# Optimization experiments

Measured on AMD Instinct MI355X. Metric: run time of the kernel, lower is better.

The kernel has to match this reference:

```python
import math
import jax, jax.numpy as jnp
from jax import lax
import numpy as np

B, S2, D = 8, 1024, 768  # seq_len = 32*32 spatial tokens
HD = 64                   # head_dim
K = 7                     # LocalRmsNorm kernel_size
EPS = 1e-7


def setup_inputs() -> dict:
    key = jax.random.key(0)
    ks = jax.random.split(key, 6)
    sc = 0.02
    return {
        "x": jax.random.normal(ks[0], (B, S2, D), jnp.float32),
        "norm_w": jnp.ones((D,), jnp.float32),
        "wq": jax.random.normal(ks[1], (D, D), jnp.float32) * sc,
        "bq": jnp.zeros((D,), jnp.float32),
        "wk": jax.random.normal(ks[2], (D, D), jnp.float32) * sc,
        "bk": jnp.zeros((D,), jnp.float32),
        "wv": jax.random.normal(ks[3], (D, D), jnp.float32) * sc,
        "bv": jnp.zeros((D,), jnp.float32),
        "wo": jax.random.normal(ks[4], (D, D), jnp.float32) * sc,
        "bo": jnp.zeros((D,), jnp.float32),
    }


def local_rms_norm(x, w):
    # x: [b, s*s, d]; sliding KxK box-sum of squares over the s x s grid,
    # zero-padded (matches F.unfold), mean divisor is always K*K.
    b, ss, d = x.shape
    s = int(math.isqrt(ss))
    sq = (x * x).reshape(b, s, s, d)
    box = lax.reduce_window(sq, 0.0, lax.add,
                            (1, K, K, 1), (1, 1, 1, 1), 'SAME')
    rms = jnp.sqrt(EPS + box / (K * K)).reshape(b, ss, d)
    return x / rms * w


def reference(x, norm_w, wq, bq, wk, bk, wv, bv, wo, bo):
    xn = local_rms_norm(x, norm_w)
    b, s, d = xn.shape
    h = d // HD

    def proj(w_, b_):
        return (xn @ w_.T + b_).reshape(b, s, h, HD).transpose(0, 2, 1, 3)

    q = proj(wq, bq)  # [b, h, s, dh]
    k = proj(wk, bk)
    v = proj(wv, bv)
    scores = jnp.einsum('bhqd,bhkd->bhqk', q, k) / math.sqrt(HD)
    attn = jax.nn.softmax(scores, axis=-1)
    out = jnp.einsum('bhqk,bhkd->bhqd', attn, v)
    out = out.transpose(0, 2, 1, 3).reshape(b, s, d)
    return out @ wo.T + bo
```

## Files before the change

kernel.cpp:

```cpp
#include <hip/hip_runtime.h>

typedef _Float16 f16x8 __attribute__((ext_vector_type(8)));
typedef _Float16 f16x4 __attribute__((ext_vector_type(4)));
typedef _Float16 f16x2 __attribute__((ext_vector_type(2)));
typedef float    f32x4 __attribute__((ext_vector_type(4)));
typedef float    f32x16 __attribute__((ext_vector_type(16)));
typedef unsigned int u32x4 __attribute__((ext_vector_type(4)));
typedef unsigned short ushort_t;
typedef unsigned int uint_t;

#define LOG2E 1.44269504088896340736f

#define CFENCE  asm volatile("" ::: "memory")
#define HWBAR   __builtin_amdgcn_s_barrier()
#define VMCNT0  asm volatile("s_waitcnt vmcnt(0)" ::: "memory")
#define VMCNT3  asm volatile("s_waitcnt vmcnt(3)" ::: "memory")
#define VMCNT4  asm volatile("s_waitcnt vmcnt(4)" ::: "memory")

__device__ __forceinline__ ushort_t f2h(float x) {
  _Float16 h = (_Float16)x;
  return __builtin_bit_cast(ushort_t, h);
}

__device__ __forceinline__ float fexp2(float x) {
#if __has_builtin(__builtin_amdgcn_exp2f)
  return __builtin_amdgcn_exp2f(x);
#else
  float r; asm("v_exp_f32 %0, %1" : "=v"(r) : "v"(x)); return r;
#endif
}

__device__ __forceinline__ float frsq(float x) {
#if __has_builtin(__builtin_amdgcn_rsqf)
  return __builtin_amdgcn_rsqf(x);
#else
  float r; asm("v_rsq_f32 %0, %1" : "=v"(r) : "v"(x)); return r;
#endif
}

__device__ __forceinline__ uint_t packpair(float a, float b) {
  return __builtin_bit_cast(uint_t, __builtin_amdgcn_cvt_pkrtz(a, b));
}

__device__ __forceinline__ f16x8 mk8(uint_t a, uint_t b, uint_t c, uint_t d) {
  u32x4 t; t[0] = a; t[1] = b; t[2] = c; t[3] = d;
  return __builtin_bit_cast(f16x8, t);
}

__device__ __forceinline__ void gload_lds16(const void* g, void* lds) {
  __builtin_amdgcn_global_load_lds(
      (const __attribute__((address_space(1))) void*)(uintptr_t)g,
      (__attribute__((address_space(3))) void*)(unsigned)(uintptr_t)lds,
      16, 0, 0);
}


__global__ __launch_bounds__(256)
void lrn_a(const float* __restrict__ x, ushort_t* __restrict__ tmp) {
  int tid = blockIdx.x * 256 + threadIdx.x;
  int dv  = tid % 192;
  int rem = tid / 192;
  int pos = rem & 1023;
  int b   = rem >> 10;
  int r = pos >> 5, c = pos & 31;
  const float4* base = (const float4*)x + ((size_t)b * 1024 + (size_t)r * 32) * 192 + dv;
  float ax = 0.f, ay = 0.f, az = 0.f, aw = 0.f;
#pragma unroll
  for (int dc = -3; dc <= 3; ++dc) {
    int cc = c + dc;
    if (cc >= 0 && cc < 32) {
      float4 v = base[cc * 192];
      ax += v.x * v.x; ay += v.y * v.y; az += v.z * v.z; aw += v.w * v.w;
    }
  }
  f16x4 o;
  o[0] = (_Float16)ax; o[1] = (_Float16)ay; o[2] = (_Float16)az; o[3] = (_Float16)aw;
  *(f16x4*)(tmp + (size_t)tid * 4) = o;
}

__global__ __launch_bounds__(256)
void lrn_b(const float* __restrict__ x, const ushort_t* __restrict__ tmp,
           const float* __restrict__ wn, ushort_t* __restrict__ xn) {
  int tid = blockIdx.x * 256 + threadIdx.x;
  int dv  = tid % 192;
  int rem = tid / 192;
  int pos = rem & 1023;
  int b   = rem >> 10;
  int r = pos >> 5, c = pos & 31;
  const ushort_t* tb = tmp + (((size_t)b * 1024 + c) * 192 + dv) * 4;
  float ax = 0.f, ay = 0.f, az = 0.f, aw = 0.f;
#pragma unroll
  for (int dr = -3; dr <= 3; ++dr) {
    int rr = r + dr;
    if (rr >= 0 && rr < 32) {
      f16x4 v = *(const f16x4*)(tb + (size_t)rr * 24576);
      ax += (float)v[0]; ay += (float)v[1]; az += (float)v[2]; aw += (float)v[3];
    }
  }
  float4 xv = ((const float4*)x)[tid];
  float4 wv = ((const float4*)wn)[dv];
  const float inv49 = 1.0f / 49.0f;
  float i0 = frsq(1e-7f + ax * inv49);
  float i1 = frsq(1e-7f + ay * inv49);
  float i2 = frsq(1e-7f + az * inv49);
  float i3 = frsq(1e-7f + aw * inv49);
  f16x4 o;
  o[0] = (_Float16)(xv.x * i0 * wv.x);
  o[1] = (_Float16)(xv.y * i1 * wv.y);
  o[2] = (_Float16)(xv.z * i2 * wv.z);
  o[3] = (_Float16)(xv.w * i3 * wv.w);
  const int m = b * 1024 + pos;
  const int panel = m >> 4, lrr = m & 15;
  const int kc = dv >> 3, lg2 = (dv >> 1) & 3, half = dv & 1;
  *(f16x4*)(xn + ((size_t)((panel * 24 + kc) * 64 + lg2 * 16 + lrr)) * 8 + half * 4) = o;
}

__global__ __launch_bounds__(256)
void convw_fm(const float* __restrict__ wq, const float* __restrict__ wk,
              const float* __restrict__ wv, const float* __restrict__ wo,
              ushort_t* __restrict__ bqkv, ushort_t* __restrict__ bwo) {
  const int g = blockIdx.x * 256 + threadIdx.x;
  const int mat = g / 73728;
  const int gg = g % 73728;
  const int panel = gg / 1536;
  const int rem = gg % 1536;
  const int kc = rem >> 6, l = rem & 63;
  const int row = panel * 16 + (l & 15);
  const int col = kc * 32 + (l >> 4) * 8;
  const float* src = (mat == 0) ? wq : (mat == 1) ? wk : (mat == 2) ? wv : wo;
  const float4 v0 = *(const float4*)(src + (size_t)row * 768 + col);
  const float4 v1 = *(const float4*)(src + (size_t)row * 768 + col + 4);
  f16x8 o;
  o[0]=(_Float16)v0.x; o[1]=(_Float16)v0.y; o[2]=(_Float16)v0.z; o[3]=(_Float16)v0.w;
  o[4]=(_Float16)v1.x; o[5]=(_Float16)v1.y; o[6]=(_Float16)v1.z; o[7]=(_Float16)v1.w;
  if (mat < 3) *(f16x8*)(bqkv + (size_t)g * 8) = o;
  else         *(f16x8*)(bwo  + (size_t)gg * 8) = o;
}

#define GSTAGE(BUF, KT) do {                                                      \
    _Pragma("unroll")                                                             \
    for (int j = 0; j < SI; ++j)                                                  \
      gload_lds16(sb[j] + (KT) * 512, (BUF) ? d1[j] : d0[j]);                     \
  } while (0)

#define GTILE(KT, CUR, NXT) do {                                                  \
    CFENCE; HWBAR; CFENCE;                              \
    if ((KT) + 1 < 24) {                                                          \
      GSTAGE(NXT, (KT) + 1);                                                      \
      if constexpr (SI == 4) VMCNT4; else VMCNT3;       \
    } else VMCNT0;                                                                \
    CFENCE; HWBAR;                                \
    __builtin_amdgcn_sched_barrier(0);                                            \
    f16x8 af[MT], bf[NT];                                                         \
    _Pragma("unroll")                                                             \
    for (int mt = 0; mt < MT; ++mt)                                               \
      af[mt] = *(const f16x8*)(&As[CUR][(wr * MT + mt) * 512 + l * 8]);           \
    _Pragma("unroll")                                                             \
    for (int nt = 0; nt < NT; ++nt)                                               \
      bf[nt] = *(const f16x8*)(&Bs[CUR][(wc * NT + nt) * 512 + l * 8]);           \
    _Pragma("unroll")                                                             \
    for (int mt = 0; mt < MT; ++mt)                                               \
      _Pragma("unroll")                                                           \
      for (int nt = 0; nt < NT; ++nt)                                             \
        acc[mt][nt] = __builtin_amdgcn_mfma_f32_16x16x32_f16(af[mt], bf[nt], acc[mt][nt], 0, 0, 0); \
  } while (0)

template <int MODE>
__global__ __launch_bounds__(256)
void gemm_lds(const ushort_t* __restrict__ Afm, const ushort_t* __restrict__ Bfm,
              const float* __restrict__ b0, const float* __restrict__ b1,
              const float* __restrict__ b2,
              ushort_t* __restrict__ q, ushort_t* __restrict__ k,
              ushort_t* __restrict__ v, float* __restrict__ outf) {
  constexpr int PM  = (MODE == 0) ? 8 : 4;
  constexpr int PN  = 8;
  constexpr int NBN = (MODE == 0) ? 18 : 6;
  constexpr int SI  = (PM + PN) / 4;
  constexpr int MT  = PM / 2, NT = PN / 2;
  __shared__ __align__(16) ushort_t As[2][PM * 512];
  __shared__ __align__(16) ushort_t Bs[2][PN * 512];

  const int nwg = gridDim.x;
  const int bid = blockIdx.x;
  const int cid = (bid & 7) * (nwg >> 3) + (bid >> 3);
  const int bm = cid / NBN, bn = cid % NBN;
  const int tid = threadIdx.x;
  const int w = tid >> 6, l = tid & 63;
  const int wr = w >> 1, wc = w & 1;
  const int lr = l & 15, lg = l >> 4;

  f32x4 acc[MT][NT] = {};

  const ushort_t* sb[SI];
  ushort_t* d0[SI];
  ushort_t* d1[SI];
#pragma unroll
  for (int j = 0; j < SI; ++j) {
    const int g = w * SI + j;
    if (g < PM) {
      sb[j] = Afm + ((size_t)(bm * PM + g) * 24) * 512 + l * 8;
      d0[j] = &As[0][g * 512]; d1[j] = &As[1][g * 512];
    } else {
      sb[j] = Bfm + ((size_t)(bn * PN + (g - PM)) * 24) * 512 + l * 8;
      d0[j] = &Bs[0][(g - PM) * 512]; d1[j] = &Bs[1][(g - PM) * 512];
    }
  }

  GSTAGE(0, 0);
  for (int kt = 0; kt < 24; kt += 2) {
    GTILE(kt, 0, 1);
    GTILE(kt + 1, 1, 0);
  }

#pragma unroll
  for (int mt = 0; mt < MT; ++mt) {
#pragma unroll
    for (int nt = 0; nt < NT; ++nt) {
      if (MODE == 0) {
        const int n = bn * 128 + wc * 64 + nt * 16 + lr;
        const int mbase = bm * 128 + wr * 64 + mt * 16 + lg * 4;
        const int region = n / 768;
        const int nn = n - region * 768;
        const int hh = nn >> 6, hd = nn & 63;
        const float bb = (region == 0 ? b0 : region == 1 ? b1 : b2)[nn];
        if (region == 2) {
          const int bi = mbase >> 10, s0 = mbase & 1023;
          const int tile = s0 >> 6, q6 = s0 & 63;
          const int aa = q6 >> 5, r5 = q6 & 31;
          const int t1 = r5 >> 3, h2 = (r5 >> 2) & 1;
          const int gq = t1 >> 1, jj = (2 * t1) & 3;
          const int s0p = (tile << 6) + (((aa << 1) + gq) << 4) + (h2 << 3) + 2 * jj;
          f16x4 pv;
#pragma unroll
          for (int gi = 0; gi < 4; ++gi) pv[gi] = (_Float16)(acc[mt][nt][gi] + bb);
          *(f16x4*)(v + (((size_t)(bi * 12 + hh)) * 64 + hd) * 1024 + s0p) = pv;
        } else {
#pragma unroll
          for (int gi = 0; gi < 4; ++gi) {
            const int m = mbase + gi;
            const int bi = m >> 10, s = m & 1023;
            const float val = acc[mt][nt][gi] + bb;
            if (region == 0)
              q[(((size_t)(bi * 12 + hh)) * 1024 + s) * 64 + hd] = f2h(val * (0.125f * LOG2E));
            else
              k[(((size_t)(bi * 12 + hh)) * 1024 + s) * 64 + hd] = f2h(val);
          }
        }
      } else {
        const int n = bn * 128 + wc * 64 + nt * 16 + lr;
        const float bb = b0[n];
#pragma unroll
        for (int gi = 0; gi < 4; ++gi) {
          const int m = bm * 64 + wr * 32 + mt * 16 + lg * 4 + gi;
          outf[(size_t)m * 768 + n] = acc[mt][nt][gi] + bb;
        }
      }
    }
  }
}

#define ATILE(T, CUR, NXT) do {                                                   \
    CFENCE; HWBAR; CFENCE;                              \
    if ((T) < 15) {                                                               \
      const int kv0n = ((T) + 1) << 6;                                            \
      gload_lds16(kp + (size_t)(kv0n + r1) * 64 + s1 * 8,  Kl0 + (NXT) * 8192);   \
      gload_lds16(kp + (size_t)(kv0n + r2) * 64 + s2 * 8,  Kl1 + (NXT) * 8192);   \
      gload_lds16(vp + (size_t)r1 * 1024 + kv0n + s1 * 8,  Vl0 + (NXT) * 8192);   \
      gload_lds16(vp + (size_t)r2 * 1024 + kv0n + s2 * 8,  Vl1 + (NXT) * 8192);   \
      VMCNT4;                                        \
    } else VMCNT0;                                                                \
    CFENCE; HWBAR;                            \
    __builtin_amdgcn_sched_barrier(0);                                            \
    const char* kbase = (const char*)smem + (CUR) * 8192;                         \
    const char* vbase = (const char*)smem + 16384 + (CUR) * 8192;                 \
    f16x8 ka0[4], ka1[4];                                                         \
    _Pragma("unroll")                                                             \
    for (int kc = 0; kc < 4; ++kc) {                                              \
      ka0[kc] = *(const f16x8*)(kbase + off[kc]);                                 \
      ka1[kc] = *(const f16x8*)(kbase + off[kc] + 4096);                          \
    }                                                                             \
    f32x16 s0v = {}, s1v = {};                                                    \
    __builtin_amdgcn_s_setprio(1);                                                \
    _Pragma("unroll")                                                             \
    for (int kc = 0; kc < 4; ++kc) {                                              \
      s0v = __builtin_amdgcn_mfma_f32_32x32x16_f16(ka0[kc], qf[kc], s0v, 0, 0, 0);\
      s1v = __builtin_amdgcn_mfma_f32_32x32x16_f16(ka1[kc], qf[kc], s1v, 0, 0, 0);\
    }                                                                             \
    __builtin_amdgcn_s_setprio(0);                                                \
    f16x8 va0[4], va1[4];                                                         \
    _Pragma("unroll")                                                             \
    for (int c = 0; c < 4; ++c) {                                                 \
      va0[c] = *(const f16x8*)(vbase + off[c]);                                   \
      va1[c] = *(const f16x8*)(vbase + off[c] + 4096);                            \
    }                                                                             \
    uint_t pk0[8], pk1[8];                                                        \
    _Pragma("unroll")                                                             \
    for (int tt = 0; tt < 8; ++tt) {                                              \
      pk0[tt] = packpair(fexp2(s0v[2 * tt]), fexp2(s0v[2 * tt + 1]));             \
      pk1[tt] = packpair(fexp2(s1v[2 * tt]), fexp2(s1v[2 * tt + 1]));             \
    }                                                                             \
    _Pragma("unroll")                                                             \
    for (int tt = 0; tt < 4; ++tt) {                                              \
      lr0 = __builtin_amdgcn_fdot2(__builtin_bit_cast(f16x2, pk0[tt]),     one2, lr0, false); \
      lr1 = __builtin_amdgcn_fdot2(__builtin_bit_cast(f16x2, pk0[tt + 4]), one2, lr1, false); \
      lr2 = __builtin_amdgcn_fdot2(__builtin_bit_cast(f16x2, pk1[tt]),     one2, lr2, false); \
      lr3 = __builtin_amdgcn_fdot2(__builtin_bit_cast(f16x2, pk1[tt + 4]), one2, lr3, false); \
    }                                                                             \
    const f16x8 pb0 = mk8(pk0[0], pk0[1], pk0[2], pk0[3]);                        \
    const f16x8 pb1 = mk8(pk0[4], pk0[5], pk0[6], pk0[7]);                        \
    const f16x8 pb2 = mk8(pk1[0], pk1[1], pk1[2], pk1[3]);                        \
    const f16x8 pb3 = mk8(pk1[4], pk1[5], pk1[6], pk1[7]);                        \
    __builtin_amdgcn_s_setprio(1);                                                \
    oacc0 = __builtin_amdgcn_mfma_f32_32x32x16_f16(va0[0], pb0, oacc0, 0, 0, 0);  \
    oacc1 = __builtin_amdgcn_mfma_f32_32x32x16_f16(va1[0], pb0, oacc1, 0, 0, 0);  \
    oacc0 = __builtin_amdgcn_mfma_f32_32x32x16_f16(va0[1], pb1, oacc0, 0, 0, 0);  \
    oacc1 = __builtin_amdgcn_mfma_f32_32x32x16_f16(va1[1], pb1, oacc1, 0, 0, 0);  \
    oacc0 = __builtin_amdgcn_mfma_f32_32x32x16_f16(va0[2], pb2, oacc0, 0, 0, 0);  \
    oacc1 = __builtin_amdgcn_mfma_f32_32x32x16_f16(va1[2], pb2, oacc1, 0, 0, 0);  \
    oacc0 = __builtin_amdgcn_mfma_f32_32x32x16_f16(va0[3], pb3, oacc0, 0, 0, 0);  \
    oacc1 = __builtin_amdgcn_mfma_f32_32x32x16_f16(va1[3], pb3, oacc1, 0, 0, 0);  \
    __builtin_amdgcn_s_setprio(0);                                                \
  } while (0)

__global__ __launch_bounds__(256, 3)
void attn_fused10(const ushort_t* __restrict__ qb, const ushort_t* __restrict__ kb,
                  const ushort_t* __restrict__ vt, ushort_t* __restrict__ ao) {
  __shared__ __align__(16) ushort_t smem[16384];
  const int tid = threadIdx.x;
  const int w = tid >> 6, l = tid & 63;
  const int lq = l & 31, hi = l >> 5;

  const int bid = blockIdx.x;
  const int cid = (bid & 7) * 96 + (bid >> 3);
  const int bh = cid >> 3, qt = cid & 7;
  const int b = bh / 12, h = bh % 12;

  const ushort_t* qp = qb + ((size_t)bh * 1024 + qt * 128 + w * 32) * 64;
  const ushort_t* kp = kb + (size_t)bh * 65536;
  const ushort_t* vp = vt + (size_t)bh * 65536;

  f16x8 qf[4];
#pragma unroll
  for (int kc = 0; kc < 4; ++kc)
    qf[kc] = *(const f16x8*)(qp + lq * 64 + kc * 16 + hi * 8);

  const int r1 = tid >> 3,          s1 = (tid & 7) ^ (r1 & 7);
  const int r2 = (tid + 256) >> 3,  s2 = (tid & 7) ^ (r2 & 7);
  char* Kl0 = (char*)smem + w * 1024;
  char* Kl1 = (char*)smem + 4096 + w * 1024;
  char* Vl0 = (char*)smem + 16384 + w * 1024;
  char* Vl1 = (char*)smem + 16384 + 4096 + w * 1024;

  const int cswz = lq & 7;
  int off[4];
#pragma unroll
  for (int kc = 0; kc < 4; ++kc)
    off[kc] = lq * 128 + (((kc * 2 + hi) ^ cswz) * 16);

  f32x16 oacc0 = {}, oacc1 = {};
  float lr0 = 0.f, lr1 = 0.f, lr2 = 0.f, lr3 = 0.f;
  const f16x2 one2 = {(_Float16)1.f, (_Float16)1.f};

  gload_lds16(kp + (size_t)r1 * 64 + s1 * 8,   Kl0);
  gload_lds16(kp + (size_t)r2 * 64 + s2 * 8,   Kl1);
  gload_lds16(vp + (size_t)r1 * 1024 + s1 * 8, Vl0);
  gload_lds16(vp + (size_t)r2 * 1024 + s2 * 8, Vl1);

  for (int t2 = 0; t2 < 16; t2 += 2) {
    ATILE(t2, 0, 1);
    ATILE(t2 + 1, 1, 0);
  }

  float lrun = (lr0 + lr1) + (lr2 + lr3);
  lrun += __shfl_xor(lrun, 32, 64);
  const float invl = 1.0f / lrun;

  __syncthreads();

  uint_t* ot = (uint_t*)smem + w * 1024 + lq * 32;
#pragma unroll
  for (int tt = 0; tt < 8; ++tt) {
    const int base = (tt & 1) + ((tt >> 1) << 2) + 2 * hi;
    ot[base ^ lq]        = packpair(oacc0[2 * tt] * invl, oacc0[2 * tt + 1] * invl);
    ot[(base + 16) ^ lq] = packpair(oacc1[2 * tt] * invl, oacc1[2 * tt + 1] * invl);
  }
  __syncthreads();
  const int row = tid >> 1, halfc = tid & 1;
  const int w2 = row >> 5, qq = row & 31;
  const uint_t* srcp = (const uint_t*)smem + w2 * 1024 + qq * 32;
  const int m = b * 1024 + qt * 128 + row;
  const int panel = m >> 4, lrr = m & 15;
  const int kc = h * 2 + halfc;
#pragma unroll
  for (int jj = 0; jj < 4; ++jj) {
    u32x4 tv;
#pragma unroll
    for (int i2 = 0; i2 < 4; ++i2)
      tv[i2] = srcp[(halfc * 16 + jj * 4 + i2) ^ qq];
    *(u32x4*)(ao + ((size_t)((panel * 24 + kc) * 64 + jj * 16 + lrr)) * 8) = tv;
  }
}

extern "C" void kernel_launch(void* const* d_in, const int* in_sizes, int n_in,
                              void* d_out, int out_size, void* d_ws, size_t ws_size,
                              hipStream_t stream) {
  const float* x  = (const float*)d_in[0];
  const float* nw = (const float*)d_in[1];
  const float* wq = (const float*)d_in[2];
  const float* bq = (const float*)d_in[3];
  const float* wk = (const float*)d_in[4];
  const float* bk = (const float*)d_in[5];
  const float* wv = (const float*)d_in[6];
  const float* bv = (const float*)d_in[7];
  const float* wo = (const float*)d_in[8];
  const float* bo = (const float*)d_in[9];
  float* out = (float*)d_out;

  char* ws = (char*)d_ws;
  ushort_t* tmp   = (ushort_t*)ws;
  ushort_t* qbuf  = (ushort_t*)(ws);
  ushort_t* kbuf  = (ushort_t*)(ws + 12582912);
  ushort_t* xnf   = (ushort_t*)(ws + 25165824);
  ushort_t* bwqkv = (ushort_t*)(ws + 37748736);
  ushort_t* bwo   = (ushort_t*)(ws + 41287680);
  ushort_t* vtb   = (ushort_t*)(ws + 42467328);
  ushort_t* aoutf = (ushort_t*)(ws + 55050240);

  lrn_a<<<6144, 256, 0, stream>>>(x, tmp);
  lrn_b<<<6144, 256, 0, stream>>>(x, tmp, nw, xnf);
  convw_fm<<<1152, 256, 0, stream>>>(wq, wk, wv, wo, bwqkv, bwo);
  gemm_lds<0><<<1152, 256, 0, stream>>>(xnf, bwqkv, bq, bk, bv,
                                        qbuf, kbuf, vtb, nullptr);
  attn_fused10<<<768, 256, 0, stream>>>(qbuf, kbuf, vtb, aoutf);
  gemm_lds<1><<<768, 256, 0, stream>>>(aoutf, bwo, bo, nullptr, nullptr,
                                       nullptr, nullptr, nullptr, out);
}
```

Baseline: 137.9 us.

## Load GEMM B operand directly into registers instead of staging through LDS

The projection GEMMs no longer stage the weight (B) tiles in shared memory. Each wave loads its own B fragments straight from global memory into double-buffered registers, while A keeps its LDS double buffer. This cuts LDS traffic and shared-memory footprint, which may let more blocks fit per CU. The cost is duplicated global reads of B across the two wave rows, more vector registers, and revised vmcnt wait counts.

```diff
diff --git a/kernel.cpp b/kernel.cpp
--- a/kernel.cpp
+++ b/kernel.cpp
@@ -14,8 +14,9 @@
 #define CFENCE  asm volatile("" ::: "memory")
 #define HWBAR   __builtin_amdgcn_s_barrier()
 #define VMCNT0  asm volatile("s_waitcnt vmcnt(0)" ::: "memory")
-#define VMCNT3  asm volatile("s_waitcnt vmcnt(3)" ::: "memory")
 #define VMCNT4  asm volatile("s_waitcnt vmcnt(4)" ::: "memory")
+#define VMCNT5  asm volatile("s_waitcnt vmcnt(5)" ::: "memory")
+#define VMCNT6  asm volatile("s_waitcnt vmcnt(6)" ::: "memory")
 
 __device__ __forceinline__ ushort_t f2h(float x) {
   _Float16 h = (_Float16)x;
@@ -137,48 +138,51 @@
   else         *(f16x8*)(bwo  + (size_t)gg * 8) = o;
 }
 
-#define GSTAGE(BUF, KT) do {                                                      \
-    _Pragma("unroll")                                                             \
-    for (int j = 0; j < SI; ++j)                                                  \
+#define GSTAGE_A(BUF, KT) do {                                                    \
+    _Pragma("unroll")                                                             \
+    for (int j = 0; j < SIA; ++j)                                                 \
       gload_lds16(sb[j] + (KT) * 512, (BUF) ? d1[j] : d0[j]);                     \
   } while (0)
 
-#define GTILE(KT, CUR, NXT) do {                                                  \
-    CFENCE; HWBAR; CFENCE;                              \
+#define GLOADB(BREG, KT) do {                                                     \
+    _Pragma("unroll")                                                             \
+    for (int nt = 0; nt < NT; ++nt)                                               \
+      BREG[nt] = *(const f16x8*)(pb[nt] + (size_t)(KT) * 512);                    \
+  } while (0)
+
+#define GTILE(KT, CUR, NXT, BCUR, BNXT) do {                                      \
+    CFENCE; HWBAR; CFENCE;                          \
     if ((KT) + 1 < 24) {                                                          \
-      GSTAGE(NXT, (KT) + 1);                                                      \
-      if constexpr (SI == 4) VMCNT4; else VMCNT3;       \
+      GSTAGE_A(NXT, (KT) + 1);                                                    \
+      GLOADB(BNXT, (KT) + 1);                                                     \
+      if constexpr (SIA == 2) VMCNT6; else VMCNT5;           \
     } else VMCNT0;                                                                \
-    CFENCE; HWBAR;                                \
+    CFENCE; HWBAR;                              \
     __builtin_amdgcn_sched_barrier(0);                                            \
-    f16x8 af[MT], bf[NT];                                                         \
+    f16x8 af[MT];                                                                 \
     _Pragma("unroll")                                                             \
     for (int mt = 0; mt < MT; ++mt)                                               \
       af[mt] = *(const f16x8*)(&As[CUR][(wr * MT + mt) * 512 + l * 8]);           \
-    _Pragma("unroll")                                                             \
-    for (int nt = 0; nt < NT; ++nt)                                               \
-      bf[nt] = *(const f16x8*)(&Bs[CUR][(wc * NT + nt) * 512 + l * 8]);           \
     _Pragma("unroll")                                                             \
     for (int mt = 0; mt < MT; ++mt)                                               \
       _Pragma("unroll")                                                           \
       for (int nt = 0; nt < NT; ++nt)                                             \
-        acc[mt][nt] = __builtin_amdgcn_mfma_f32_16x16x32_f16(af[mt], bf[nt], acc[mt][nt], 0, 0, 0); \
+        acc[mt][nt] = __builtin_amdgcn_mfma_f32_16x16x32_f16(af[mt], BCUR[nt], acc[mt][nt], 0, 0, 0); \
   } while (0)
 
 template <int MODE>
 __global__ __launch_bounds__(256)
-void gemm_lds(const ushort_t* __restrict__ Afm, const ushort_t* __restrict__ Bfm,
-              const float* __restrict__ b0, const float* __restrict__ b1,
-              const float* __restrict__ b2,
-              ushort_t* __restrict__ q, ushort_t* __restrict__ k,
-              ushort_t* __restrict__ v, float* __restrict__ outf) {
+void gemm_breg(const ushort_t* __restrict__ Afm, const ushort_t* __restrict__ Bfm,
+               const float* __restrict__ b0, const float* __restrict__ b1,
+               const float* __restrict__ b2,
+               ushort_t* __restrict__ q, ushort_t* __restrict__ k,
+               ushort_t* __restrict__ v, float* __restrict__ outf) {
   constexpr int PM  = (MODE == 0) ? 8 : 4;
   constexpr int PN  = 8;
   constexpr int NBN = (MODE == 0) ? 18 : 6;
-  constexpr int SI  = (PM + PN) / 4;
+  constexpr int SIA = PM / 4;
   constexpr int MT  = PM / 2, NT = PN / 2;
   __shared__ __align__(16) ushort_t As[2][PM * 512];
-  __shared__ __align__(16) ushort_t Bs[2][PN * 512];
 
   const int nwg = gridDim.x;
   const int bid = blockIdx.x;
@@ -191,25 +195,26 @@
 
   f32x4 acc[MT][NT] = {};
 
-  const ushort_t* sb[SI];
-  ushort_t* d0[SI];
-  ushort_t* d1[SI];
-#pragma unroll
-  for (int j = 0; j < SI; ++j) {
-    const int g = w * SI + j;
-    if (g < PM) {
-      sb[j] = Afm + ((size_t)(bm * PM + g) * 24) * 512 + l * 8;
-      d0[j] = &As[0][g * 512]; d1[j] = &As[1][g * 512];
-    } else {
-      sb[j] = Bfm + ((size_t)(bn * PN + (g - PM)) * 24) * 512 + l * 8;
-      d0[j] = &Bs[0][(g - PM) * 512]; d1[j] = &Bs[1][(g - PM) * 512];
-    }
-  }
-
-  GSTAGE(0, 0);
+  const ushort_t* sb[SIA];
+  ushort_t* d0[SIA];
+  ushort_t* d1[SIA];
+#pragma unroll
+  for (int j = 0; j < SIA; ++j) {
+    const int g = w * SIA + j;
+    sb[j] = Afm + ((size_t)(bm * PM + g) * 24) * 512 + l * 8;
+    d0[j] = &As[0][g * 512]; d1[j] = &As[1][g * 512];
+  }
+  const ushort_t* pb[NT];
+#pragma unroll
+  for (int nt = 0; nt < NT; ++nt)
+    pb[nt] = Bfm + ((size_t)(bn * PN + wc * NT + nt) * 24) * 512 + l * 8;
+
+  f16x8 bfA[NT], bfB[NT];
+  GSTAGE_A(0, 0);
+  GLOADB(bfA, 0);
   for (int kt = 0; kt < 24; kt += 2) {
-    GTILE(kt, 0, 1);
-    GTILE(kt + 1, 1, 0);
+    GTILE(kt, 0, 1, bfA, bfB);
+    GTILE(kt + 1, 1, 0, bfB, bfA);
   }
 
 #pragma unroll
@@ -429,9 +434,9 @@
   lrn_a<<<6144, 256, 0, stream>>>(x, tmp);
   lrn_b<<<6144, 256, 0, stream>>>(x, tmp, nw, xnf);
   convw_fm<<<1152, 256, 0, stream>>>(wq, wk, wv, wo, bwqkv, bwo);
-  gemm_lds<0><<<1152, 256, 0, stream>>>(xnf, bwqkv, bq, bk, bv,
-                                        qbuf, kbuf, vtb, nullptr);
+  gemm_breg<0><<<1152, 256, 0, stream>>>(xnf, bwqkv, bq, bk, bv,
+                                         qbuf, kbuf, vtb, nullptr);
   attn_fused10<<<768, 256, 0, stream>>>(qbuf, kbuf, vtb, aoutf);
-  gemm_lds<1><<<768, 256, 0, stream>>>(aoutf, bwo, bo, nullptr, nullptr,
-                                       nullptr, nullptr, nullptr, out);
-}
+  gemm_breg<1><<<768, 256, 0, stream>>>(aoutf, bwo, bo, nullptr, nullptr,
+                                        nullptr, nullptr, nullptr, out);
+}
```

Result: slower. 148.7 us (+7.8%).

## Pre-swizzle Q/K/V into MFMA fragment order in the QKV GEMM epilogue

Applied to the files above, without the earlier changes.

The QKV projection epilogue now writes Q, K and V directly in the per-lane MFMA fragment order the attention kernel consumes. Each K/V tile becomes one contiguous 8KB block, so the attention kernel can copy it linearly into LDS and read fragments with plain lane-strided loads. This removes the XOR-swizzle address math and the strided V gathers. In exchange, the epilogue stores become more scattered at 2-byte granularity for Q/K, which could slow the GEMM.

```diff
diff --git a/kernel.cpp b/kernel.cpp
--- a/kernel.cpp
+++ b/kernel.cpp
@@ -223,27 +223,36 @@
         const int nn = n - region * 768;
         const int hh = nn >> 6, hd = nn & 63;
         const float bb = (region == 0 ? b0 : region == 1 ? b1 : b2)[nn];
+        const int khalf = (hd >> 3) & 1, kch = hd >> 4, jd = hd & 7;
         if (region == 2) {
           const int bi = mbase >> 10, s0 = mbase & 1023;
           const int tile = s0 >> 6, q6 = s0 & 63;
           const int aa = q6 >> 5, r5 = q6 & 31;
           const int t1 = r5 >> 3, h2 = (r5 >> 2) & 1;
           const int gq = t1 >> 1, jj = (2 * t1) & 3;
-          const int s0p = (tile << 6) + (((aa << 1) + gq) << 4) + (h2 << 3) + 2 * jj;
+          const int chunk = (aa << 1) + gq;
+          const int gidx = (hd >> 5) * 4 + chunk;
+          const int lane = (hd & 31) + 32 * h2;
           f16x4 pv;
 #pragma unroll
           for (int gi = 0; gi < 4; ++gi) pv[gi] = (_Float16)(acc[mt][nt][gi] + bb);
-          *(f16x4*)(v + (((size_t)(bi * 12 + hh)) * 64 + hd) * 1024 + s0p) = pv;
+          *(f16x4*)(v + (((size_t)(bi * 12 + hh) * 16 + tile) * 8 + gidx) * 512
+                      + lane * 8 + 2 * jj) = pv;
         } else {
 #pragma unroll
           for (int gi = 0; gi < 4; ++gi) {
             const int m = mbase + gi;
             const int bi = m >> 10, s = m & 1023;
             const float val = acc[mt][nt][gi] + bb;
-            if (region == 0)
-              q[(((size_t)(bi * 12 + hh)) * 1024 + s) * 64 + hd] = f2h(val * (0.125f * LOG2E));
-            else
-              k[(((size_t)(bi * 12 + hh)) * 1024 + s) * 64 + hd] = f2h(val);
+            if (region == 0) {
+              const int lane = (s & 31) + 32 * khalf;
+              q[(((size_t)(bi * 12 + hh) * 32 + (s >> 5)) * 4 + kch) * 512
+                + lane * 8 + jd] = f2h(val * (0.125f * LOG2E));
+            } else {
+              const int lane = (s & 31) + 32 * khalf;
+              k[(((size_t)(bi * 12 + hh) * 16 + (s >> 6)) * 8
+                 + ((s >> 5) & 1) * 4 + kch) * 512 + lane * 8 + jd] = f2h(val);
+            }
           }
         }
       } else {
@@ -262,11 +271,12 @@
 #define ATILE(T, CUR, NXT) do {                                                   \
     CFENCE; HWBAR; CFENCE;                              \
     if ((T) < 15) {                                                               \
-      const int kv0n = ((T) + 1) << 6;                                            \
-      gload_lds16(kp + (size_t)(kv0n + r1) * 64 + s1 * 8,  Kl0 + (NXT) * 8192);   \
-      gload_lds16(kp + (size_t)(kv0n + r2) * 64 + s2 * 8,  Kl1 + (NXT) * 8192);   \
-      gload_lds16(vp + (size_t)r1 * 1024 + kv0n + s1 * 8,  Vl0 + (NXT) * 8192);   \
-      gload_lds16(vp + (size_t)r2 * 1024 + kv0n + s2 * 8,  Vl1 + (NXT) * 8192);   \
+      const ushort_t* ksrc = kp + (size_t)((T) + 1) * 4096;                       \
+      const ushort_t* vsrc = vp + (size_t)((T) + 1) * 4096;                       \
+      gload_lds16(ksrc + tid * 8,           Kl0 + (NXT) * 8192);                  \
+      gload_lds16(ksrc + (tid + 256) * 8,   Kl1 + (NXT) * 8192);                  \
+      gload_lds16(vsrc + tid * 8,           Vl0 + (NXT) * 8192);                  \
+      gload_lds16(vsrc + (tid + 256) * 8,   Vl1 + (NXT) * 8192);                  \
       VMCNT4;                                        \
     } else VMCNT0;                                                                \
     CFENCE; HWBAR;                            \
@@ -276,8 +286,8 @@
     f16x8 ka0[4], ka1[4];                                                         \
     _Pragma("unroll")                                                             \
     for (int kc = 0; kc < 4; ++kc) {                                              \
-      ka0[kc] = *(const f16x8*)(kbase + off[kc]);                                 \
-      ka1[kc] = *(const f16x8*)(kbase + off[kc] + 4096);                          \
+      ka0[kc] = *(const f16x8*)(kbase + kc * 1024 + l * 16);                      \
+      ka1[kc] = *(const f16x8*)(kbase + 4096 + kc * 1024 + l * 16);               \
     }                                                                             \
     f32x16 s0v = {}, s1v = {};                                                    \
     __builtin_amdgcn_s_setprio(1);                                                \
@@ -290,8 +300,8 @@
     f16x8 va0[4], va1[4];                                                         \
     _Pragma("unroll")                                                             \
     for (int c = 0; c < 4; ++c) {                                                 \
-      va0[c] = *(const f16x8*)(vbase + off[c]);                                   \
-      va1[c] = *(const f16x8*)(vbase + off[c] + 4096);                            \
+      va0[c] = *(const f16x8*)(vbase + c * 1024 + l * 16);                        \
+      va1[c] = *(const f16x8*)(vbase + 4096 + c * 1024 + l * 16);                 \
     }                                                                             \
     uint_t pk0[8], pk1[8];                                                        \
     _Pragma("unroll")                                                             \
@@ -323,7 +333,7 @@
   } while (0)
 
 __global__ __launch_bounds__(256, 3)
-void attn_fused10(const ushort_t* __restrict__ qb, const ushort_t* __restrict__ kb,
+void attn_fused11(const ushort_t* __restrict__ qb, const ushort_t* __restrict__ kb,
                   const ushort_t* __restrict__ vt, ushort_t* __restrict__ ao) {
   __shared__ __align__(16) ushort_t smem[16384];
   const int tid = threadIdx.x;
@@ -335,36 +345,28 @@
   const int bh = cid >> 3, qt = cid & 7;
   const int b = bh / 12, h = bh % 12;
 
-  const ushort_t* qp = qb + ((size_t)bh * 1024 + qt * 128 + w * 32) * 64;
+  const ushort_t* qp = qb + ((size_t)(bh * 32 + qt * 4 + w)) * 2048;
   const ushort_t* kp = kb + (size_t)bh * 65536;
   const ushort_t* vp = vt + (size_t)bh * 65536;
 
   f16x8 qf[4];
 #pragma unroll
   for (int kc = 0; kc < 4; ++kc)
-    qf[kc] = *(const f16x8*)(qp + lq * 64 + kc * 16 + hi * 8);
-
-  const int r1 = tid >> 3,          s1 = (tid & 7) ^ (r1 & 7);
-  const int r2 = (tid + 256) >> 3,  s2 = (tid & 7) ^ (r2 & 7);
+    qf[kc] = *(const f16x8*)(qp + kc * 512 + l * 8);
+
   char* Kl0 = (char*)smem + w * 1024;
   char* Kl1 = (char*)smem + 4096 + w * 1024;
   char* Vl0 = (char*)smem + 16384 + w * 1024;
   char* Vl1 = (char*)smem + 16384 + 4096 + w * 1024;
 
-  const int cswz = lq & 7;
-  int off[4];
-#pragma unroll
-  for (int kc = 0; kc < 4; ++kc)
-    off[kc] = lq * 128 + (((kc * 2 + hi) ^ cswz) * 16);
-
   f32x16 oacc0 = {}, oacc1 = {};
   float lr0 = 0.f, lr1 = 0.f, lr2 = 0.f, lr3 = 0.f;
   const f16x2 one2 = {(_Float16)1.f, (_Float16)1.f};
 
-  gload_lds16(kp + (size_t)r1 * 64 + s1 * 8,   Kl0);
-  gload_lds16(kp + (size_t)r2 * 64 + s2 * 8,   Kl1);
-  gload_lds16(vp + (size_t)r1 * 1024 + s1 * 8, Vl0);
-  gload_lds16(vp + (size_t)r2 * 1024 + s2 * 8, Vl1);
+  gload_lds16(kp + tid * 8,         Kl0);
+  gload_lds16(kp + (tid + 256) * 8, Kl1);
+  gload_lds16(vp + tid * 8,         Vl0);
+  gload_lds16(vp + (tid + 256) * 8, Vl1);
 
   for (int t2 = 0; t2 < 16; t2 += 2) {
     ATILE(t2, 0, 1);
@@ -431,7 +433,7 @@
   convw_fm<<<1152, 256, 0, stream>>>(wq, wk, wv, wo, bwqkv, bwo);
   gemm_lds<0><<<1152, 256, 0, stream>>>(xnf, bwqkv, bq, bk, bv,
                                         qbuf, kbuf, vtb, nullptr);
-  attn_fused10<<<768, 256, 0, stream>>>(qbuf, kbuf, vtb, aoutf);
+  attn_fused11<<<768, 256, 0, stream>>>(qbuf, kbuf, vtb, aoutf);
   gemm_lds<1><<<768, 256, 0, stream>>>(aoutf, bwo, bo, nullptr, nullptr,
                                        nullptr, nullptr, nullptr, out);
 }
```

Result: no change. 135.6 us (-1.7%).
